# Optimization experiments

Hardware: AMD Instinct MI355X
Metric: run time of the kernel (lower is better)

The kernel has to match this reference:

```python
import jax, jax.numpy as jnp
import numpy as np

B, T, DKQ, DV, EKQ, EV, H, OUT = 8, 2048, 64, 64, 128, 128, 4, 32
FF = 4 * EV
NEG = -1e30  # additive mask value (safe stand-in for -inf)


def _ln(x, g, b, eps=1e-5):
    m = x.mean(-1, keepdims=True)
    var = ((x - m) ** 2).mean(-1, keepdims=True)
    return (x - m) * jax.lax.rsqrt(var + eps) * g + b


def _attn(q, k, v, mask):
    # q,k,v: [n, T, E] -> heads [n, H, T, dh]; NOTE: no 1/sqrt(d) scaling (faithful to source)
    n, t, _ = q.shape
    q = q.reshape(n, t, H, -1).transpose(0, 2, 1, 3)
    k = k.reshape(n, t, H, -1).transpose(0, 2, 1, 3)
    v = v.reshape(n, t, H, -1).transpose(0, 2, 1, 3)
    w = jnp.einsum('bhqd,bhkd->bhqk', q, k) + mask  # [n,H,T,T]
    a = jax.nn.softmax(w, axis=-1)
    o = jnp.einsum('bhqk,bhkd->bhqd', a, v)
    return o.transpose(0, 2, 1, 3).reshape(n, t, -1)


def setup_inputs() -> dict:
    key = jax.random.key(0)
    ks = jax.random.split(key, 32)
    w = lambda k, s: jax.random.normal(k, s, jnp.float32) * 0.02
    DIN_A = DKQ + DV
    return {
        'kq': jax.random.normal(ks[0], (B, T, DKQ), jnp.float32),
        'v': jax.random.normal(ks[1], (B, T, DV), jnp.float32),
        # Layer A (input_dim = DKQ+DV, embed = EV)
        'A_Wk': w(ks[2], (DIN_A, EV)), 'A_bk': jnp.zeros((EV,), jnp.float32),
        'A_Wq': w(ks[3], (DIN_A, EV)), 'A_bq': jnp.zeros((EV,), jnp.float32),
        'A_Wv': w(ks[4], (DIN_A, EV)), 'A_bv': jnp.zeros((EV,), jnp.float32),
        'A_f1W': w(ks[5], (EV, FF)), 'A_f1b': jnp.zeros((FF,), jnp.float32),
        'A_f2W': w(ks[6], (FF, EV)), 'A_f2b': jnp.zeros((EV,), jnp.float32),
        'A_n1g': jnp.ones((EV,), jnp.float32), 'A_n1b': jnp.zeros((EV,), jnp.float32),
        'A_n2g': jnp.ones((EV,), jnp.float32), 'A_n2b': jnp.zeros((EV,), jnp.float32),
        # Layer B (kq -> EKQ, vA -> EV)
        'B_Wk': w(ks[7], (DKQ, EKQ)), 'B_bk': jnp.zeros((EKQ,), jnp.float32),
        'B_Wq': w(ks[8], (DKQ, EKQ)), 'B_bq': jnp.zeros((EKQ,), jnp.float32),
        'B_Wv': w(ks[9], (EV, EV)), 'B_bv': jnp.zeros((EV,), jnp.float32),
        'B_f1W': w(ks[10], (EV, FF)), 'B_f1b': jnp.zeros((FF,), jnp.float32),
        'B_f2W': w(ks[11], (FF, EV)), 'B_f2b': jnp.zeros((EV,), jnp.float32),
        # Output head
        'out_W': w(ks[12], (EV, OUT)), 'out_b': jnp.zeros((OUT,), jnp.float32),
    }


def reference(kq, v, A_Wk, A_bk, A_Wq, A_bq, A_Wv, A_bv, A_f1W, A_f1b, A_f2W, A_f2b,
              A_n1g, A_n1b, A_n2g, A_n2b, B_Wk, B_bk, B_Wq, B_bq, B_Wv, B_bv,
              B_f1W, B_f1b, B_f2W, B_f2b, out_W, out_b):
    n, t, _ = kq.shape
    i = jnp.arange(t)[:, None]
    j = jnp.arange(t)[None, :]
    mask_a = jnp.where(j <= i, 0.0, NEG).astype(jnp.float32)               # causal (diag=1)
    mask_b = jnp.where((j < i) | ((i == 0) & (j == 0)), 0.0, NEG).astype(jnp.float32)  # strict causal + (0,0) exception

    # ---- Layer A ----
    X = jnp.concatenate([kq, v], axis=-1)
    K = X @ A_Wk + A_bk
    Q = X @ A_Wq + A_bq
    V = X @ A_Wv + A_bv
    attn_out = _attn(Q, K, V, mask_a)
    h1 = _ln(V + attn_out, A_n1g, A_n1b)
    ff = jax.nn.gelu(h1 @ A_f1W + A_f1b, approximate=False) @ A_f2W + A_f2b
    vA = _ln(h1 + ff, A_n2g, A_n2b)

    # ---- Layer B (no residuals / norms: values is overwritten in source) ----
    K2 = kq @ B_Wk + B_bk
    Q2 = kq @ B_Wq + B_bq
    V2 = vA @ B_Wv + B_bv
    attn_out2 = _attn(Q2, K2, V2, mask_b)
    ff2 = jax.nn.gelu(attn_out2 @ B_f1W + B_f1b, approximate=False) @ B_f2W + B_f2b

    return ff2 @ out_W + out_b
```

## Files before the change

### kernel.cpp

```cpp
#include <hip/hip_runtime.h>
#include <hip/hip_bf16.h>
#include <type_traits>

#define TSEQ 2048
#define NBATCH 8
#define NROWS (NBATCH*TSEQ)
#define EMB 128
#define NH 4
#define DH 32
#define OUTD 32
#define APLANE (NROWS*EMB)
#define LOG2E 1.44269504088896340736f
#define NPAR 4

typedef short s8v __attribute__((ext_vector_type(8)));
typedef short s4v __attribute__((ext_vector_type(4)));
typedef float f4v __attribute__((ext_vector_type(4)));
typedef float f16v __attribute__((ext_vector_type(16)));
typedef unsigned int u4v __attribute__((ext_vector_type(4)));

__device__ __forceinline__ unsigned short f2bf(float f){
  unsigned int u = __float_as_uint(f);
  unsigned int r = u + 0x7fffu + ((u >> 16) & 1u);
  return (unsigned short)(r >> 16);
}
__device__ __forceinline__ float bf2f(unsigned short u){
  return __uint_as_float(((unsigned int)u) << 16);
}
__device__ __forceinline__ float exp2fast(float x){
#if __has_builtin(__builtin_amdgcn_exp2f)
  return __builtin_amdgcn_exp2f(x);
#else
  return __expf(x * 0.6931471805599453f);
#endif
}

struct WPack {
  const float* src[10];
  int off[10];
  int ntk[10];
  int rowoff[10];
  int nsh[10];
  int kn[10];
};
__global__ __launch_bounds__(256) void prep(WPack p, short* __restrict__ warena,
                                            const float* __restrict__ kq, const float* __restrict__ v,
                                            unsigned short* __restrict__ X){
  int blk = blockIdx.x;
  if (blk < (NROWS*EMB/256)){
    int idx = blk*256 + threadIdx.x;
    int row = idx >> 7, c = idx & 127;
    float val = (c < 64) ? kq[row*64 + c] : v[row*64 + (c-64)];
    unsigned short hi = f2bf(val);
    X[idx]          = hi;
    X[idx + APLANE] = f2bf(val - bf2f(hi));
    return;
  }
  blk -= (NROWS*EMB/256);
  int m = 0;
  #pragma unroll
  for (int i=0;i<10;i++){
    int nb = p.kn[i] >> 8;
    if (blk < nb){ m = i; break; }
    blk -= nb;
  }
  int idx = blk*256 + threadIdx.x;
  float x = p.src[m][idx];
  int nsh = p.nsh[m];
  int n = idx & ((1<<nsh)-1);
  int k = idx >> nsh;
  int K = p.kn[m] >> nsh;
  unsigned short hi = f2bf(x);
  unsigned short lo = f2bf(x - bf2f(hi));
  short* dh = warena + p.off[m] + (size_t)(p.rowoff[m] + n)*K + k;
  dh[0]        = (short)hi;
  dh[p.ntk[m]] = (short)lo;
}

struct GOuts {
  const float* bias[3];
  float* of[3];
  unsigned short* ob[3];
  float scl[3];
};
template<int CT, int NWV, int NITER, int CB>
__global__ __launch_bounds__(NWV*64) void gemm2(
    const unsigned short* __restrict__ A, int aplane, int lda, int K,
    const short* __restrict__ wt, int NTK,
    GOuts og, int NT, int nseg, int act,
    unsigned short* __restrict__ vtb, int vcol0,
    const float* __restrict__ cbO, const float* __restrict__ cbL){
  __shared__ short As[2][2][64*40];
  const int tid  = threadIdx.x;
  const int w    = tid >> 6;
  const int lane = tid & 63;
  const int col  = lane & 15;
  const int quad = lane >> 4;
  const int row0 = blockIdx.x * 64;
  const int cb   = blockIdx.y*(NWV*16*CT) + w*(16*CT) + col;
  const bool two = CB ? true : (aplane != 0);

  f4v acc[4][CT];
  #pragma unroll
  for (int i=0;i<4;i++)
    #pragma unroll
    for (int j=0;j<CT;j++) acc[i][j] = (f4v){0.f,0.f,0.f,0.f};

  using sv = typename std::conditional<NWV==4, s8v, s4v>::type;
  const int ar = (NWV==4) ? (tid >> 2) : (tid >> 3);
  const int ac = (NWV==4) ? ((tid & 3)*8) : ((tid & 7)*4);

  const unsigned short* abase = nullptr;
  sv pah, pal;
  float4 cnx[NPAR]; float cnl[NPAR];
  if constexpr (CB){
    #pragma unroll
    for (int p2=0;p2<NPAR;p2++){
      cnx[p2] = *(const float4*)(cbO + (size_t)p2*NROWS*EMB + (size_t)(row0+ar)*EMB + ac);
      cnl[p2] = cbL[(size_t)p2*NROWS*NH + (size_t)(row0+ar)*NH + 0];
    }
  } else {
    abase = A + (size_t)(row0 + ar)*lda;
    pah = *(const sv*)(abase + ac);
    if (two) pal = *(const sv*)(abase + aplane + ac);
  }

  const short* wbase[CT];
  #pragma unroll
  for (int ct=0;ct<CT;ct++) wbase[ct] = wt + (size_t)(cb + ct*16)*K + quad*8;

  s8v wh[CT], wl[CT], wnh[CT], wnl[CT];
  #pragma unroll
  for (int ct=0;ct<CT;ct++){
    wh[ct] = *(const s8v*)(wbase[ct]);
    wl[ct] = *(const s8v*)(wbase[ct] + NTK);
  }

  #pragma unroll
  for (int i=0;i<NITER;i++){
    const int buf = i & 1;
    if constexpr (CB){
      float sx=0.f, sy=0.f, sz=0.f, sw=0.f, ls=0.f;
      #pragma unroll
      for (int p2=0;p2<NPAR;p2++){
        sx += cnx[p2].x; sy += cnx[p2].y; sz += cnx[p2].z; sw += cnx[p2].w;
        ls += cnl[p2];
      }
      const float linv = 1.f/ls;
      float xs[4] = {sx*linv, sy*linv, sz*linv, sw*linv};
      s4v ph, pl;
      #pragma unroll
      for (int j=0;j<4;j++){
        unsigned short hb = f2bf(xs[j]);
        ph[j] = (short)hb;
        pl[j] = (short)f2bf(xs[j] - bf2f(hb));
      }
      *(s4v*)&As[buf][0][ar*40 + ac] = ph;
      *(s4v*)&As[buf][1][ar*40 + ac] = pl;
    } else {
      *(sv*)&As[buf][0][ar*40 + ac] = pah;
      if (two) *(sv*)&As[buf][1][ar*40 + ac] = pal;
    }
    __syncthreads();
    if (i+1 < NITER){
      if constexpr (CB){
        #pragma unroll
        for (int p2=0;p2<NPAR;p2++){
          cnx[p2] = *(const float4*)(cbO + (size_t)p2*NROWS*EMB + (size_t)(row0+ar)*EMB + (i+1)*32 + ac);
          cnl[p2] = cbL[(size_t)p2*NROWS*NH + (size_t)(row0+ar)*NH + (i+1)];
        }
      } else {
        const int kcol = (i+1)*32 + ac;
        pah = *(const sv*)(abase + kcol);
        if (two) pal = *(const sv*)(abase + aplane + kcol);
      }
      #pragma unroll
      for (int ct=0;ct<CT;ct++){
        wnh[ct] = *(const s8v*)(wbase[ct] + (i+1)*32);
        wnl[ct] = *(const s8v*)(wbase[ct] + (i+1)*32 + NTK);
      }
    }
    #pragma unroll
    for (int rt=0;rt<4;rt++){
      s8v ah = *(const s8v*)&As[buf][0][(rt*16 + col)*40 + quad*8];
      #pragma unroll
      for (int ct=0;ct<CT;ct++)
        acc[rt][ct] = __builtin_amdgcn_mfma_f32_16x16x32_bf16(ah, wh[ct], acc[rt][ct], 0, 0, 0);
      if (two){
        s8v al = *(const s8v*)&As[buf][1][(rt*16 + col)*40 + quad*8];
        #pragma unroll
        for (int ct=0;ct<CT;ct++)
          acc[rt][ct] = __builtin_amdgcn_mfma_f32_16x16x32_bf16(al, wh[ct], acc[rt][ct], 0, 0, 0);
      }
      #pragma unroll
      for (int ct=0;ct<CT;ct++)
        acc[rt][ct] = __builtin_amdgcn_mfma_f32_16x16x32_bf16(ah, wl[ct], acc[rt][ct], 0, 0, 0);
    }
    if (i+1 < NITER){
      #pragma unroll
      for (int ct=0;ct<CT;ct++){ wh[ct] = wnh[ct]; wl[ct] = wnl[ct]; }
    }
  }

  const int NB = NWV*16*CT;
  const int cb0 = (int)blockIdx.y * NB;
  const bool dotr = (NB == 128) && (vtb != nullptr) && (cb0 >= vcol0) && (cb0 < vcol0 + 128);
  short* Lt = &As[0][0][0];
  if (dotr) __syncthreads();

  #pragma unroll
  for (int ct=0;ct<CT;ct++){
    const int cg = cb + ct*16;
    int seg, lcol, ldc;
    if (nseg > 1){ seg = cg >> 7; lcol = cg & 127; ldc = 128; }
    else         { seg = 0; lcol = cg; ldc = NT; }
    const float bv = og.bias[seg][lcol];
    const float sc = og.scl[seg];
    float* of = og.of[seg];
    unsigned short* ob = og.ob[seg];
    #pragma unroll
    for (int rt=0;rt<4;rt++){
      s4v pk;
      #pragma unroll
      for (int r=0;r<4;r++){
        const int row = row0 + rt*16 + quad*4 + r;
        float val = acc[rt][ct][r] + bv;
        if (act == 1) val = 0.5f*val*(1.f + erff(val*0.70710678118654752440f));
        val *= sc;
        if (ob)      ob[(size_t)row*ldc + lcol] = f2bf(val);
        else if (of) of[(size_t)row*ldc + lcol] = val;
        if (dotr) pk[r] = (short)f2bf(val);
      }
      if (dotr)
        *(s4v*)&Lt[((cg - cb0))*72 + rt*16 + quad*4] = pk;
    }
  }
  if (dotr){
    __syncthreads();
    const int b = row0 >> 11, t0 = row0 & 2047;
    #pragma unroll
    for (int it=0; it<2*CT; it++){
      const int cl = it*(NWV*8) + (tid>>3);
      const int t8 = (tid&7)*8;
      s8v o = *(const s8v*)&Lt[cl*72 + t8];
      const int cr = cb0 + cl - vcol0;
      *(s8v*)(vtb + ((size_t)((b*4 + (cr>>5))*32 + (cr&31)))*2048 + t0 + t8) = o;
    }
  }
}

template<int MODE>
__global__ __launch_bounds__(512) void gemm_f2(
    const unsigned short* __restrict__ A,
    const short* __restrict__ wt, int NTK,
    const float* __restrict__ bias,
    const unsigned short* __restrict__ resid,
    const float* __restrict__ g, const float* __restrict__ bt,
    unsigned short* __restrict__ outp,
    const float* __restrict__ Wo, const float* __restrict__ bo,
    float* __restrict__ outhead){
  __shared__ short As[2][64*40];
  __shared__ float Lf[64*132];
  __shared__ float Ws2[128*32];
  const int tid  = threadIdx.x;
  const int w    = tid >> 6;
  const int lane = tid & 63;
  const int col  = lane & 15;
  const int quad = lane >> 4;
  const int row0 = blockIdx.x * 64;
  const int cg   = w*16 + col;

  if (MODE == 1){
    for (int idx = tid; idx < 128*32; idx += 512) Ws2[idx] = Wo[idx];
  }

  f4v acc[4];
  #pragma unroll
  for (int i=0;i<4;i++) acc[i] = (f4v){0.f,0.f,0.f,0.f};

  const int ar = tid >> 3, ac = (tid & 7)*4;
  const unsigned short* abase = A + (size_t)(row0 + ar)*512;
  s4v pa = *(const s4v*)(abase + ac);
  const short* wb = wt + (size_t)cg*512 + quad*8;

  for (int i=0;i<16;i++){
    const int buf = i & 1;
    *(s4v*)&As[buf][ar*40 + ac] = pa;
    __syncthreads();
    if (i+1 < 16) pa = *(const s4v*)(abase + (i+1)*32 + ac);
    s8v bh = *(const s8v*)(wb + i*32);
    s8v bl = *(const s8v*)(wb + i*32 + NTK);
    #pragma unroll
    for (int rt=0;rt<4;rt++){
      s8v ah = *(const s8v*)&As[buf][(rt*16 + col)*40 + quad*8];
      acc[rt] = __builtin_amdgcn_mfma_f32_16x16x32_bf16(ah, bh, acc[rt], 0, 0, 0);
      acc[rt] = __builtin_amdgcn_mfma_f32_16x16x32_bf16(ah, bl, acc[rt], 0, 0, 0);
    }
  }

  const float bv = bias[cg];
  #pragma unroll
  for (int rt=0;rt<4;rt++){
    #pragma unroll
    for (int r=0;r<4;r++){
      const int row = rt*16 + quad*4 + r;
      Lf[row*132 + cg] = acc[rt][r] + bv;
    }
  }
  __syncthreads();

  if (MODE == 0){
    for (int rr=0; rr<8; rr++){
      const int row = w*8 + rr;
      const size_t gbase = (size_t)(row0 + row)*EMB;
      float x0 = Lf[row*132 + lane]
               + bf2f(resid[gbase+lane])    + bf2f(resid[gbase+lane+APLANE]);
      float x1 = Lf[row*132 + lane + 64]
               + bf2f(resid[gbase+lane+64]) + bf2f(resid[gbase+lane+64+APLANE]);
      float s  = x0 + x1;
      float s2 = x0*x0 + x1*x1;
      #pragma unroll
      for (int off=1; off<64; off<<=1){
        s  += __shfl_xor(s,  off);
        s2 += __shfl_xor(s2, off);
      }
      float mean = s * (1.f/128.f);
      float var  = s2 * (1.f/128.f) - mean*mean;
      float rstd = rsqrtf(var + 1e-5f);
      float y0 = (x0-mean)*rstd*g[lane]    + bt[lane];
      float y1 = (x1-mean)*rstd*g[lane+64] + bt[lane+64];
      unsigned short h0b = f2bf(y0), h1b = f2bf(y1);
      outp[gbase+lane]             = h0b;
      outp[gbase+lane+64]          = h1b;
      outp[gbase+lane+APLANE]      = f2bf(y0 - bf2f(h0b));
      outp[gbase+lane+64+APLANE]   = f2bf(y1 - bf2f(h1b));
    }
  } else {
    const int row = tid >> 3, c0 = (tid & 7)*4;
    f4v a4;
    #pragma unroll
    for (int j=0;j<4;j++) a4[j] = bo[c0+j];
    #pragma unroll 16
    for (int k=0;k<128;k++){
      const float av = Lf[row*132 + k];
      #pragma unroll
      for (int j=0;j<4;j++) a4[j] = fmaf(av, Ws2[k*32 + c0 + j], a4[j]);
    }
    float* op = outhead + (size_t)(row0 + row)*OUTD + c0;
    #pragma unroll
    for (int j=0;j<4;j++) op[j] = a4[j];
  }
}

#define KSTR 40
#define VSTR 72
__device__ __forceinline__ int kswz(int row, int c){ return (row*KSTR + c) ^ (((row>>3)&3)<<3); }
__device__ __forceinline__ int vswz(int row, int c){ return (row*VSTR + c) ^ (((row>>3)&3)<<3); }

__global__ __launch_bounds__(256, 4) void flash5(const unsigned short* __restrict__ Qb,
                                                 const unsigned short* __restrict__ Kb,
                                                 const unsigned short* __restrict__ Vtb,
                                                 float* __restrict__ O, float* __restrict__ L,
                                                 int mode){
  __shared__ short Kt[64*KSTR];
  __shared__ short Vt[32*VSTR];
  const int tid  = threadIdx.x;
  const int w    = tid >> 6;
  const int lane = tid & 63;
  const int q31  = lane & 31;
  const int hi   = lane >> 5;
  const int bh = blockIdx.y;
  const int b = bh >> 2, h = bh & 3;
  const int par = blockIdx.z;
  float* Op = O + (size_t)par*NROWS*EMB;
  float* Lp = L + (size_t)par*NROWS*NH;
  const int kr = tid >> 2, kc8 = (tid & 3)*8;
  const int vd = tid >> 3, vk8 = (tid & 7)*8;

  for (int pass = 0; pass < 2; pass++){
    const int qt = pass ? (int)blockIdx.x : (15 - (int)blockIdx.x);
    const int qbase = qt*128;
    const int qrow  = qbase + w*32 + q31;
    const int jtmax = 2*qt + 1;

    s8v qB0 = *(const s8v*)(Qb + (size_t)(b*TSEQ + qrow)*EMB + h*DH + hi*8);
    s8v qB1 = *(const s8v*)(Qb + (size_t)(b*TSEQ + qrow)*EMB + h*DH + 16 + hi*8);
    f16v o;
    #pragma unroll
    for (int r=0;r<16;r++) o[r] = 0.f;
    float lr = 0.f;

    if (par <= jtmax){
      s8v ka = *(const s8v*)(Kb + (size_t)(b*TSEQ + par*64 + kr)*EMB + h*DH + kc8);
      s8v va = *(const s8v*)(Vtb + ((size_t)bh*32 + vd)*TSEQ + par*64 + vk8);
      for (int jt = par; jt <= jtmax; jt += NPAR){
        __syncthreads();
        *(s8v*)&Kt[kswz(kr, kc8)] = ka;
        *(s8v*)&Vt[vswz(vd, vk8)] = va;
        __syncthreads();
        if (jt + NPAR <= jtmax){
          ka = *(const s8v*)(Kb + (size_t)(b*TSEQ + (jt+NPAR)*64 + kr)*EMB + h*DH + kc8);
          va = *(const s8v*)(Vtb + ((size_t)bh*32 + vd)*TSEQ + (jt+NPAR)*64 + vk8);
        }
        const bool domask = (jt >= 2*qt);
        #pragma unroll
        for (int kt=0;kt<2;kt++){
          f16v s;
          #pragma unroll
          for (int r=0;r<16;r++) s[r] = 0.f;
          {
            s8v kf0 = *(const s8v*)&Kt[kswz(kt*32 + q31, hi*8)];
            s = __builtin_amdgcn_mfma_f32_32x32x16_bf16(kf0, qB0, s, 0, 0, 0);
            s8v kf1 = *(const s8v*)&Kt[kswz(kt*32 + q31, 16 + hi*8)];
            s = __builtin_amdgcn_mfma_f32_32x32x16_bf16(kf1, qB1, s, 0, 0, 0);
          }
          if (domask){
            #pragma unroll
            for (int r=0;r<16;r++){
              const int jg = jt*64 + kt*32 + (r&3) + 8*(r>>2) + 4*hi;
              const bool ok = (mode==0) ? (jg <= qrow) : ((jg < qrow) || (qrow==0 && jg==0));
              s[r] = ok ? s[r] : -1e30f;
            }
          }
          #pragma unroll
          for (int r=0;r<16;r++){ float pv = exp2fast(s[r]); s[r] = pv; lr += pv; }
          unsigned P2[4][2];
          #pragma unroll
          for (int m=0;m<4;m++){
            asm("v_cvt_pk_bf16_f32 %0, %1, %2" : "=v"(P2[m][0]) : "v"(s[4*m+0]), "v"(s[4*m+1]));
            asm("v_cvt_pk_bf16_f32 %0, %1, %2" : "=v"(P2[m][1]) : "v"(s[4*m+2]), "v"(s[4*m+3]));
          }
          #pragma unroll
          for (int kcl=0;kcl<2;kcl++){
            const unsigned own0 = hi ? P2[2*kcl+1][0] : P2[2*kcl][0];
            const unsigned own1 = hi ? P2[2*kcl+1][1] : P2[2*kcl][1];
            const unsigned inv0 = hi ? P2[2*kcl][0]   : P2[2*kcl+1][0];
            const unsigned inv1 = hi ? P2[2*kcl][1]   : P2[2*kcl+1][1];
            const unsigned sx0 = (unsigned)__shfl_xor((int)inv0, 32);
            const unsigned sx1 = (unsigned)__shfl_xor((int)inv1, 32);
            u4v au;
            au[0] = hi ? sx0 : own0;  au[1] = hi ? sx1 : own1;
            au[2] = hi ? own0 : sx0;  au[3] = hi ? own1 : sx1;
            s8v af = __builtin_bit_cast(s8v, au);
            s8v vf = *(const s8v*)&Vt[vswz(q31, kt*32 + kcl*16 + hi*8)];
            o = __builtin_amdgcn_mfma_f32_32x32x16_bf16(af, vf, o, 0, 0, 0);
          }
        }
      }
    }
    const float lt = lr + __shfl_xor(lr, 32);
    #pragma unroll
    for (int r=0;r<16;r++){
      const int ql = (r&3) + 8*(r>>2) + 4*hi;
      Op[(size_t)(b*TSEQ + qbase + w*32 + ql)*EMB + h*DH + q31] = o[r];
    }
    if (hi == 0) Lp[(size_t)(b*TSEQ + qrow)*NH + h] = lt;
  }
}

__global__ __launch_bounds__(256) void combine_ln(const float* __restrict__ O, const float* __restrict__ L,
                                                  const float* __restrict__ Vf,
                                                  const float* __restrict__ g, const float* __restrict__ bt,
                                                  unsigned short* __restrict__ outp){
  const int row = blockIdx.x*4 + (threadIdx.x >> 6);
  const int tid = threadIdx.x & 63;
  const size_t base = (size_t)row*EMB;
  const int h0 = tid >> 5, h1i = 2 + (tid >> 5);
  float la = 0.f, lb = 0.f, s0 = 0.f, s1 = 0.f;
  #pragma unroll
  for (int p=0;p<NPAR;p++){
    la += L[(size_t)p*NROWS*NH + (size_t)row*NH + h0];
    lb += L[(size_t)p*NROWS*NH + (size_t)row*NH + h1i];
    s0 += O[(size_t)p*NROWS*EMB + base + tid];
    s1 += O[(size_t)p*NROWS*EMB + base + tid + 64];
  }
  float x0 = Vf[base+tid]    + s0/la;
  float x1 = Vf[base+tid+64] + s1/lb;
  float s  = x0 + x1;
  float s2 = x0*x0 + x1*x1;
  #pragma unroll
  for (int off=1; off<64; off<<=1){
    s  += __shfl_xor(s,  off);
    s2 += __shfl_xor(s2, off);
  }
  float mean = s * (1.f/128.f);
  float var  = s2 * (1.f/128.f) - mean*mean;
  float rstd = rsqrtf(var + 1e-5f);
  float y0 = (x0-mean)*rstd*g[tid]    + bt[tid];
  float y1 = (x1-mean)*rstd*g[tid+64] + bt[tid+64];
  unsigned short h0b = f2bf(y0), h1b = f2bf(y1);
  outp[base+tid]             = h0b;
  outp[base+tid+64]          = h1b;
  outp[base+tid+APLANE]      = f2bf(y0 - bf2f(h0b));
  outp[base+tid+64+APLANE]   = f2bf(y1 - bf2f(h1b));
}

extern "C" void kernel_launch(void* const* d_in, const int* in_sizes, int n_in,
                              void* d_out, int out_size, void* d_ws, size_t ws_size,
                              hipStream_t stream) {
  const float* kq    = (const float*)d_in[0];
  const float* v     = (const float*)d_in[1];
  const float* A_Wk  = (const float*)d_in[2];  const float* A_bk  = (const float*)d_in[3];
  const float* A_Wq  = (const float*)d_in[4];  const float* A_bq  = (const float*)d_in[5];
  const float* A_Wv  = (const float*)d_in[6];  const float* A_bv  = (const float*)d_in[7];
  const float* A_f1W = (const float*)d_in[8];  const float* A_f1b = (const float*)d_in[9];
  const float* A_f2W = (const float*)d_in[10]; const float* A_f2b = (const float*)d_in[11];
  const float* A_n1g = (const float*)d_in[12]; const float* A_n1b = (const float*)d_in[13];
  const float* A_n2g = (const float*)d_in[14]; const float* A_n2b = (const float*)d_in[15];
  const float* B_Wk  = (const float*)d_in[16]; const float* B_bk  = (const float*)d_in[17];
  const float* B_Wq  = (const float*)d_in[18]; const float* B_bq  = (const float*)d_in[19];
  const float* B_Wv  = (const float*)d_in[20]; const float* B_bv  = (const float*)d_in[21];
  const float* B_f1W = (const float*)d_in[22]; const float* B_f1b = (const float*)d_in[23];
  const float* B_f2W = (const float*)d_in[24]; const float* B_f2b = (const float*)d_in[25];
  const float* out_W = (const float*)d_in[26]; const float* out_b = (const float*)d_in[27];
  float* out = (float*)d_out;
  (void)in_sizes; (void)n_in; (void)out_size; (void)ws_size;

  char* ws = (char*)d_ws;
  const size_t MB = 1024*1024;
  short* warena = (short*)ws;
  unsigned short* Xs  = (unsigned short*)(ws + 2*MB);
  unsigned short* Qbf = (unsigned short*)(ws + 10*MB);
  unsigned short* Kbf = (unsigned short*)(ws + 14*MB);
  unsigned short* Vtb = (unsigned short*)(ws + 18*MB);
  float* Vf  = (float*)(ws + 22*MB);
  float* Opar = (float*)(ws + 30*MB);
  float* Lpar = (float*)(ws + 62*MB);
  unsigned short* h1p = (unsigned short*)(ws + 66*MB);
  unsigned short* mid = (unsigned short*)(ws + 74*MB);
  unsigned short* vAp = (unsigned short*)(ws + 90*MB);

  WPack p;
  const float* srcs[10] = {A_Wq,A_Wk,A_Wv,A_f1W,A_f2W,B_Wq,B_Wk,B_Wv,B_f1W,B_f2W};
  int kn[10]     = {16384,16384,16384,65536,65536,8192,8192,16384,65536,65536};
  int nsh[10]    = {7,7,7,9,7,7,7,7,9,7};
  int off[10]    = {0,0,0,98304,229376,360448,360448,393216,425984,557056};
  int ntk[10]    = {49152,49152,49152,65536,65536,16384,16384,16384,65536,65536};
  int rowoff[10] = {0,128,256,0,0,0,128,0,0,0};
  int nblk = 0;
  for (int i=0;i<10;i++){
    p.src[i]=srcs[i]; p.kn[i]=kn[i]; p.nsh[i]=nsh[i];
    p.off[i]=off[i]; p.ntk[i]=ntk[i]; p.rowoff[i]=rowoff[i];
    nblk += kn[i] >> 8;
  }
  prep<<<(NROWS*EMB/256) + nblk, 256, 0, stream>>>(p, warena, kq, v, Xs);

  GOuts oQKVA = {{A_bq,A_bk,A_bv},{nullptr,nullptr,Vf},{Qbf,Kbf,nullptr},{LOG2E,1.f,1.f}};
  GOuts oF1A  = {{A_f1b,nullptr,nullptr},{nullptr,nullptr,nullptr},{mid,nullptr,nullptr},{1.f,1.f,1.f}};
  GOuts oQKB  = {{B_bq,B_bk,nullptr},{nullptr,nullptr,nullptr},{Qbf,Kbf,nullptr},{LOG2E,1.f,1.f}};
  GOuts oVB   = {{B_bv,nullptr,nullptr},{nullptr,nullptr,nullptr},{nullptr,nullptr,nullptr},{1.f,1.f,1.f}};
  GOuts oF1B  = {{B_f1b,nullptr,nullptr},{nullptr,nullptr,nullptr},{mid,nullptr,nullptr},{1.f,1.f,1.f}};

  gemm2<2,4,4,0><<<dim3(256,3), 256, 0, stream>>>(Xs, APLANE, 128, 128, warena + 0, 49152, oQKVA, 384, 3, 0, Vtb, 256, nullptr, nullptr);
  flash5<<<dim3(8,32,NPAR), 256, 0, stream>>>(Qbf, Kbf, Vtb, Opar, Lpar, 0);
  combine_ln<<<NROWS/4, 256, 0, stream>>>(Opar, Lpar, Vf, A_n1g, A_n1b, h1p);
  gemm2<2,8,4,0><<<dim3(256,2), 512, 0, stream>>>(h1p, APLANE, 128, 128, warena + 98304, 65536, oF1A, 512, 1, 1, nullptr, 0, nullptr, nullptr);
  gemm_f2<0><<<256, 512, 0, stream>>>(mid, warena + 229376, 65536, A_f2b,
                                      h1p, A_n2g, A_n2b, vAp, nullptr, nullptr, nullptr);

  gemm2<2,8,2,0><<<dim3(256,1), 512, 0, stream>>>(Xs, APLANE, 128, 64, warena + 360448, 16384, oQKB, 256, 2, 0, nullptr, 0, nullptr, nullptr);
  gemm2<1,8,4,0><<<dim3(256,1), 512, 0, stream>>>(vAp, APLANE, 128, 128, warena + 393216, 16384, oVB, 128, 1, 0, Vtb, 0, nullptr, nullptr);
  flash5<<<dim3(8,32,NPAR), 256, 0, stream>>>(Qbf, Kbf, Vtb, Opar, Lpar, 1);
  gemm2<2,8,4,1><<<dim3(256,2), 512, 0, stream>>>(nullptr, 1, 128, 128, warena + 425984, 65536, oF1B, 512, 1, 1, nullptr, 0, Opar, Lpar);
  gemm_f2<1><<<256, 512, 0, stream>>>(mid, warena + 557056, 65536, B_f2b,
                                      nullptr, nullptr, nullptr, nullptr, out_W, out_b, out);
}
```

Measured before the change: 274.3 us.

## Fuse attention combine+LayerNorm into FF1 GEMM and merge QKV launches

Removes the separate combine_ln kernel by computing the partial-attention combine, residual add and LayerNorm inside the FF1 GEMM prologue (new CB==2 mode), with the by==0 blocks also writing h1 for the later residual. It also merges layer A's QKV GEMM and layer B's QK GEMM into a single launch, using separate Q/K buffers so layer B's projections don't overwrite layer A's. This cuts two kernel launches and one round trip of h1 through memory. The cost is that both column blocks of the FF1 GEMM redundantly redo the combine and LayerNorm reads, and register pressure in the prologue goes up.

```diff
diff --git a/kernel.cpp b/kernel.cpp
--- a/kernel.cpp
+++ b/kernel.cpp
@@ -83,22 +83,26 @@
   unsigned short* ob[3];
   float scl[3];
 };
+struct GArgs {
+  const unsigned short* A; int aplane; int lda; int K;
+  const short* wt; int NTK;
+  GOuts og; int NT; int nseg; int act;
+  unsigned short* vtb; int vcol0;
+  const float* cbO; const float* cbL;
+  const float* vf; const float* lng; const float* lnb;
+  unsigned short* h1out;
+};
+
 template<int CT, int NWV, int NITER, int CB>
-__global__ __launch_bounds__(NWV*64) void gemm2(
-    const unsigned short* __restrict__ A, int aplane, int lda, int K,
-    const short* __restrict__ wt, int NTK,
-    GOuts og, int NT, int nseg, int act,
-    unsigned short* __restrict__ vtb, int vcol0,
-    const float* __restrict__ cbO, const float* __restrict__ cbL){
-  __shared__ short As[2][2][64*40];
+__device__ __forceinline__ void gemm2_body(short* __restrict__ AsD, const GArgs a, int bx, int by){
   const int tid  = threadIdx.x;
   const int w    = tid >> 6;
   const int lane = tid & 63;
   const int col  = lane & 15;
   const int quad = lane >> 4;
-  const int row0 = blockIdx.x * 64;
-  const int cb   = blockIdx.y*(NWV*16*CT) + w*(16*CT) + col;
-  const bool two = CB ? true : (aplane != 0);
+  const int row0 = bx * 64;
+  const int cb   = by*(NWV*16*CT) + w*(16*CT) + col;
+  const bool two = (CB != 0) ? true : (a.aplane != 0);
 
   f4v acc[4][CT];
   #pragma unroll
@@ -113,33 +117,69 @@
   const unsigned short* abase = nullptr;
   sv pah, pal;
   float4 cnx[NPAR]; float cnl[NPAR];
-  if constexpr (CB){
+  float x[16];
+  if constexpr (CB == 1){
     #pragma unroll
     for (int p2=0;p2<NPAR;p2++){
-      cnx[p2] = *(const float4*)(cbO + (size_t)p2*NROWS*EMB + (size_t)(row0+ar)*EMB + ac);
-      cnl[p2] = cbL[(size_t)p2*NROWS*NH + (size_t)(row0+ar)*NH + 0];
-    }
+      cnx[p2] = *(const float4*)(a.cbO + (size_t)p2*NROWS*EMB + (size_t)(row0+ar)*EMB + ac);
+      cnl[p2] = a.cbL[(size_t)p2*NROWS*NH + (size_t)(row0+ar)*NH + 0];
+    }
+  } else if constexpr (CB == 2){
+    float s = 0.f, s2 = 0.f;
+    #pragma unroll
+    for (int i=0;i<NITER;i++){
+      float sx=0.f, sy=0.f, sz=0.f, sw=0.f, ls=0.f;
+      #pragma unroll
+      for (int p2=0;p2<NPAR;p2++){
+        float4 t = *(const float4*)(a.cbO + (size_t)p2*NROWS*EMB + (size_t)(row0+ar)*EMB + i*32 + ac);
+        sx += t.x; sy += t.y; sz += t.z; sw += t.w;
+        ls += a.cbL[(size_t)p2*NROWS*NH + (size_t)(row0+ar)*NH + i];
+      }
+      float4 vv = *(const float4*)(a.vf + (size_t)(row0+ar)*EMB + i*32 + ac);
+      const float linv = 1.f/ls;
+      x[i*4+0] = vv.x + sx*linv;
+      x[i*4+1] = vv.y + sy*linv;
+      x[i*4+2] = vv.z + sz*linv;
+      x[i*4+3] = vv.w + sw*linv;
+      #pragma unroll
+      for (int j=0;j<4;j++){ s += x[i*4+j]; s2 += x[i*4+j]*x[i*4+j]; }
+    }
+    #pragma unroll
+    for (int off=1; off<8; off<<=1){
+      s  += __shfl_xor(s,  off);
+      s2 += __shfl_xor(s2, off);
+    }
+    const float mean = s * (1.f/128.f);
+    const float var  = s2 * (1.f/128.f) - mean*mean;
+    const float rstd = rsqrtf(var + 1e-5f);
+    #pragma unroll
+    for (int i=0;i<NITER;i++)
+      #pragma unroll
+      for (int j=0;j<4;j++){
+        const int cg2 = i*32 + ac + j;
+        x[i*4+j] = (x[i*4+j]-mean)*rstd*a.lng[cg2] + a.lnb[cg2];
+      }
   } else {
-    abase = A + (size_t)(row0 + ar)*lda;
+    abase = a.A + (size_t)(row0 + ar)*a.lda;
     pah = *(const sv*)(abase + ac);
-    if (two) pal = *(const sv*)(abase + aplane + ac);
+    if (two) pal = *(const sv*)(abase + a.aplane + ac);
   }
 
   const short* wbase[CT];
   #pragma unroll
-  for (int ct=0;ct<CT;ct++) wbase[ct] = wt + (size_t)(cb + ct*16)*K + quad*8;
+  for (int ct=0;ct<CT;ct++) wbase[ct] = a.wt + (size_t)(cb + ct*16)*a.K + quad*8;
 
   s8v wh[CT], wl[CT], wnh[CT], wnl[CT];
   #pragma unroll
   for (int ct=0;ct<CT;ct++){
     wh[ct] = *(const s8v*)(wbase[ct]);
-    wl[ct] = *(const s8v*)(wbase[ct] + NTK);
+    wl[ct] = *(const s8v*)(wbase[ct] + a.NTK);
   }
 
   #pragma unroll
   for (int i=0;i<NITER;i++){
     const int buf = i & 1;
-    if constexpr (CB){
+    if constexpr (CB == 1){
       float sx=0.f, sy=0.f, sz=0.f, sw=0.f, ls=0.f;
       #pragma unroll
       for (int p2=0;p2<NPAR;p2++){
@@ -155,39 +195,53 @@
         ph[j] = (short)hb;
         pl[j] = (short)f2bf(xs[j] - bf2f(hb));
       }
-      *(s4v*)&As[buf][0][ar*40 + ac] = ph;
-      *(s4v*)&As[buf][1][ar*40 + ac] = pl;
+      *(s4v*)&AsD[(buf*2+0)*2560 + ar*40 + ac] = ph;
+      *(s4v*)&AsD[(buf*2+1)*2560 + ar*40 + ac] = pl;
+    } else if constexpr (CB == 2){
+      s4v ph, pl;
+      #pragma unroll
+      for (int j=0;j<4;j++){
+        unsigned short hb = f2bf(x[i*4+j]);
+        ph[j] = (short)hb;
+        pl[j] = (short)f2bf(x[i*4+j] - bf2f(hb));
+      }
+      *(s4v*)&AsD[(buf*2+0)*2560 + ar*40 + ac] = ph;
+      *(s4v*)&AsD[(buf*2+1)*2560 + ar*40 + ac] = pl;
+      if (by == 0 && a.h1out){
+        *(s4v*)(a.h1out + (size_t)(row0+ar)*EMB + i*32 + ac) = ph;
+        *(s4v*)(a.h1out + APLANE + (size_t)(row0+ar)*EMB + i*32 + ac) = pl;
+      }
     } else {
-      *(sv*)&As[buf][0][ar*40 + ac] = pah;
-      if (two) *(sv*)&As[buf][1][ar*40 + ac] = pal;
+      *(sv*)&AsD[(buf*2+0)*2560 + ar*40 + ac] = pah;
+      if (two) *(sv*)&AsD[(buf*2+1)*2560 + ar*40 + ac] = pal;
     }
     __syncthreads();
     if (i+1 < NITER){
-      if constexpr (CB){
+      if constexpr (CB == 1){
         #pragma unroll
         for (int p2=0;p2<NPAR;p2++){
-          cnx[p2] = *(const float4*)(cbO + (size_t)p2*NROWS*EMB + (size_t)(row0+ar)*EMB + (i+1)*32 + ac);
-          cnl[p2] = cbL[(size_t)p2*NROWS*NH + (size_t)(row0+ar)*NH + (i+1)];
+          cnx[p2] = *(const float4*)(a.cbO + (size_t)p2*NROWS*EMB + (size_t)(row0+ar)*EMB + (i+1)*32 + ac);
+          cnl[p2] = a.cbL[(size_t)p2*NROWS*NH + (size_t)(row0+ar)*NH + (i+1)];
         }
-      } else {
+      } else if constexpr (CB == 0){
         const int kcol = (i+1)*32 + ac;
         pah = *(const sv*)(abase + kcol);
-        if (two) pal = *(const sv*)(abase + aplane + kcol);
+        if (two) pal = *(const sv*)(abase + a.aplane + kcol);
       }
       #pragma unroll
       for (int ct=0;ct<CT;ct++){
         wnh[ct] = *(const s8v*)(wbase[ct] + (i+1)*32);
-        wnl[ct] = *(const s8v*)(wbase[ct] + (i+1)*32 + NTK);
+        wnl[ct] = *(const s8v*)(wbase[ct] + (i+1)*32 + a.NTK);
       }
     }
     #pragma unroll
     for (int rt=0;rt<4;rt++){
-      s8v ah = *(const s8v*)&As[buf][0][(rt*16 + col)*40 + quad*8];
+      s8v ah = *(const s8v*)&AsD[(buf*2+0)*2560 + (rt*16 + col)*40 + quad*8];
       #pragma unroll
       for (int ct=0;ct<CT;ct++)
         acc[rt][ct] = __builtin_amdgcn_mfma_f32_16x16x32_bf16(ah, wh[ct], acc[rt][ct], 0, 0, 0);
       if (two){
-        s8v al = *(const s8v*)&As[buf][1][(rt*16 + col)*40 + quad*8];
+        s8v al = *(const s8v*)&AsD[(buf*2+1)*2560 + (rt*16 + col)*40 + quad*8];
         #pragma unroll
         for (int ct=0;ct<CT;ct++)
           acc[rt][ct] = __builtin_amdgcn_mfma_f32_16x16x32_bf16(al, wh[ct], acc[rt][ct], 0, 0, 0);
@@ -203,21 +257,21 @@
   }
 
   const int NB = NWV*16*CT;
-  const int cb0 = (int)blockIdx.y * NB;
-  const bool dotr = (NB == 128) && (vtb != nullptr) && (cb0 >= vcol0) && (cb0 < vcol0 + 128);
-  short* Lt = &As[0][0][0];
+  const int cb0 = by * NB;
+  const bool dotr = (NB == 128) && (a.vtb != nullptr) && (cb0 >= a.vcol0) && (cb0 < a.vcol0 + 128);
+  short* Lt = AsD;
   if (dotr) __syncthreads();
 
   #pragma unroll
   for (int ct=0;ct<CT;ct++){
     const int cg = cb + ct*16;
     int seg, lcol, ldc;
-    if (nseg > 1){ seg = cg >> 7; lcol = cg & 127; ldc = 128; }
-    else         { seg = 0; lcol = cg; ldc = NT; }
-    const float bv = og.bias[seg][lcol];
-    const float sc = og.scl[seg];
-    float* of = og.of[seg];
-    unsigned short* ob = og.ob[seg];
+    if (a.nseg > 1){ seg = cg >> 7; lcol = cg & 127; ldc = 128; }
+    else           { seg = 0; lcol = cg; ldc = a.NT; }
+    const float bv = a.og.bias[seg][lcol];
+    const float sc = a.og.scl[seg];
+    float* of = a.og.of[seg];
+    unsigned short* ob = a.og.ob[seg];
     #pragma unroll
     for (int rt=0;rt<4;rt++){
       s4v pk;
@@ -225,7 +279,7 @@
       for (int r=0;r<4;r++){
         const int row = row0 + rt*16 + quad*4 + r;
         float val = acc[rt][ct][r] + bv;
-        if (act == 1) val = 0.5f*val*(1.f + erff(val*0.70710678118654752440f));
+        if (a.act == 1) val = 0.5f*val*(1.f + erff(val*0.70710678118654752440f));
         val *= sc;
         if (ob)      ob[(size_t)row*ldc + lcol] = f2bf(val);
         else if (of) of[(size_t)row*ldc + lcol] = val;
@@ -243,10 +297,22 @@
       const int cl = it*(NWV*8) + (tid>>3);
       const int t8 = (tid&7)*8;
       s8v o = *(const s8v*)&Lt[cl*72 + t8];
-      const int cr = cb0 + cl - vcol0;
-      *(s8v*)(vtb + ((size_t)((b*4 + (cr>>5))*32 + (cr&31)))*2048 + t0 + t8) = o;
-    }
-  }
+      const int cr = cb0 + cl - a.vcol0;
+      *(s8v*)(a.vtb + ((size_t)((b*4 + (cr>>5))*32 + (cr&31)))*2048 + t0 + t8) = o;
+    }
+  }
+}
+
+template<int CT, int NWV, int NITER, int CB>
+__global__ __launch_bounds__(NWV*64) void gemm2k(GArgs a){
+  extern __shared__ short AsD[];
+  gemm2_body<CT,NWV,NITER,CB>(AsD, a, blockIdx.x, blockIdx.y);
+}
+
+__global__ __launch_bounds__(256) void gemm_mixa(GArgs qkva, GArgs qkb){
+  extern __shared__ short AsD[];
+  if (blockIdx.y < 3) gemm2_body<2,4,4,0>(AsD, qkva, blockIdx.x, blockIdx.y);
+  else                gemm2_body<2,4,2,0>(AsD, qkb,  blockIdx.x, blockIdx.y - 3);
 }
 
 template<int MODE>
@@ -458,43 +524,6 @@
   }
 }
 
-__global__ __launch_bounds__(256) void combine_ln(const float* __restrict__ O, const float* __restrict__ L,
-                                                  const float* __restrict__ Vf,
-                                                  const float* __restrict__ g, const float* __restrict__ bt,
-                                                  unsigned short* __restrict__ outp){
-  const int row = blockIdx.x*4 + (threadIdx.x >> 6);
-  const int tid = threadIdx.x & 63;
-  const size_t base = (size_t)row*EMB;
-  const int h0 = tid >> 5, h1i = 2 + (tid >> 5);
-  float la = 0.f, lb = 0.f, s0 = 0.f, s1 = 0.f;
-  #pragma unroll
-  for (int p=0;p<NPAR;p++){
-    la += L[(size_t)p*NROWS*NH + (size_t)row*NH + h0];
-    lb += L[(size_t)p*NROWS*NH + (size_t)row*NH + h1i];
-    s0 += O[(size_t)p*NROWS*EMB + base + tid];
-    s1 += O[(size_t)p*NROWS*EMB + base + tid + 64];
-  }
-  float x0 = Vf[base+tid]    + s0/la;
-  float x1 = Vf[base+tid+64] + s1/lb;
-  float s  = x0 + x1;
-  float s2 = x0*x0 + x1*x1;
-  #pragma unroll
-  for (int off=1; off<64; off<<=1){
-    s  += __shfl_xor(s,  off);
-    s2 += __shfl_xor(s2, off);
-  }
-  float mean = s * (1.f/128.f);
-  float var  = s2 * (1.f/128.f) - mean*mean;
-  float rstd = rsqrtf(var + 1e-5f);
-  float y0 = (x0-mean)*rstd*g[tid]    + bt[tid];
-  float y1 = (x1-mean)*rstd*g[tid+64] + bt[tid+64];
-  unsigned short h0b = f2bf(y0), h1b = f2bf(y1);
-  outp[base+tid]             = h0b;
-  outp[base+tid+64]          = h1b;
-  outp[base+tid+APLANE]      = f2bf(y0 - bf2f(h0b));
-  outp[base+tid+64+APLANE]   = f2bf(y1 - bf2f(h1b));
-}
-
 extern "C" void kernel_launch(void* const* d_in, const int* in_sizes, int n_in,
                               void* d_out, int out_size, void* d_ws, size_t ws_size,
                               hipStream_t stream) {
@@ -529,6 +558,8 @@
   unsigned short* h1p = (unsigned short*)(ws + 66*MB);
   unsigned short* mid = (unsigned short*)(ws + 74*MB);
   unsigned short* vAp = (unsigned short*)(ws + 90*MB);
+  unsigned short* Qb2 = (unsigned short*)(ws + 98*MB);
+  unsigned short* Kb2 = (unsigned short*)(ws + 102*MB);
 
   WPack p;
   const float* srcs[10] = {A_Wq,A_Wk,A_Wv,A_f1W,A_f2W,B_Wq,B_Wk,B_Wv,B_f1W,B_f2W};
@@ -547,21 +578,27 @@
 
   GOuts oQKVA = {{A_bq,A_bk,A_bv},{nullptr,nullptr,Vf},{Qbf,Kbf,nullptr},{LOG2E,1.f,1.f}};
   GOuts oF1A  = {{A_f1b,nullptr,nullptr},{nullptr,nullptr,nullptr},{mid,nullptr,nullptr},{1.f,1.f,1.f}};
-  GOuts oQKB  = {{B_bq,B_bk,nullptr},{nullptr,nullptr,nullptr},{Qbf,Kbf,nullptr},{LOG2E,1.f,1.f}};
+  GOuts oQKB  = {{B_bq,B_bk,nullptr},{nullptr,nullptr,nullptr},{Qb2,Kb2,nullptr},{LOG2E,1.f,1.f}};
   GOuts oVB   = {{B_bv,nullptr,nullptr},{nullptr,nullptr,nullptr},{nullptr,nullptr,nullptr},{1.f,1.f,1.f}};
   GOuts oF1B  = {{B_f1b,nullptr,nullptr},{nullptr,nullptr,nullptr},{mid,nullptr,nullptr},{1.f,1.f,1.f}};
 
-  gemm2<2,4,4,0><<<dim3(256,3), 256, 0, stream>>>(Xs, APLANE, 128, 128, warena + 0, 49152, oQKVA, 384, 3, 0, Vtb, 256, nullptr, nullptr);
+  const int SH = 2*2*64*40*(int)sizeof(short);
+
+  GArgs aQKVA = {Xs, APLANE, 128, 128, warena + 0,      49152, oQKVA, 384, 3, 0, Vtb, 256, nullptr, nullptr, nullptr, nullptr, nullptr, nullptr};
+  GArgs aQKB  = {Xs, APLANE, 128, 64,  warena + 360448, 16384, oQKB,  256, 2, 0, nullptr, 0, nullptr, nullptr, nullptr, nullptr, nullptr, nullptr};
+  GArgs aF1A  = {nullptr, 1, 128, 128, warena + 98304,  65536, oF1A,  512, 1, 1, nullptr, 0, Opar, Lpar, Vf, A_n1g, A_n1b, h1p};
+  GArgs aVB   = {vAp, APLANE, 128, 128, warena + 393216, 16384, oVB,  128, 1, 0, Vtb, 0, nullptr, nullptr, nullptr, nullptr, nullptr, nullptr};
+  GArgs aF1B  = {nullptr, 1, 128, 128, warena + 425984,  65536, oF1B,  512, 1, 1, nullptr, 0, Opar, Lpar, nullptr, nullptr, nullptr, nullptr};
+
+  gemm_mixa<<<dim3(256,5), 256, SH, stream>>>(aQKVA, aQKB);
   flash5<<<dim3(8,32,NPAR), 256, 0, stream>>>(Qbf, Kbf, Vtb, Opar, Lpar, 0);
-  combine_ln<<<NROWS/4, 256, 0, stream>>>(Opar, Lpar, Vf, A_n1g, A_n1b, h1p);
-  gemm2<2,8,4,0><<<dim3(256,2), 512, 0, stream>>>(h1p, APLANE, 128, 128, warena + 98304, 65536, oF1A, 512, 1, 1, nullptr, 0, nullptr, nullptr);
+  gemm2k<2,8,4,2><<<dim3(256,2), 512, SH, stream>>>(aF1A);
   gemm_f2<0><<<256, 512, 0, stream>>>(mid, warena + 229376, 65536, A_f2b,
                                       h1p, A_n2g, A_n2b, vAp, nullptr, nullptr, nullptr);
 
-  gemm2<2,8,2,0><<<dim3(256,1), 512, 0, stream>>>(Xs, APLANE, 128, 64, warena + 360448, 16384, oQKB, 256, 2, 0, nullptr, 0, nullptr, nullptr);
-  gemm2<1,8,4,0><<<dim3(256,1), 512, 0, stream>>>(vAp, APLANE, 128, 128, warena + 393216, 16384, oVB, 128, 1, 0, Vtb, 0, nullptr, nullptr);
-  flash5<<<dim3(8,32,NPAR), 256, 0, stream>>>(Qbf, Kbf, Vtb, Opar, Lpar, 1);
-  gemm2<2,8,4,1><<<dim3(256,2), 512, 0, stream>>>(nullptr, 1, 128, 128, warena + 425984, 65536, oF1B, 512, 1, 1, nullptr, 0, Opar, Lpar);
+  gemm2k<1,8,4,0><<<dim3(256,1), 512, SH, stream>>>(aVB);
+  flash5<<<dim3(8,32,NPAR), 256, 0, stream>>>(Qb2, Kb2, Vtb, Opar, Lpar, 1);
+  gemm2k<2,8,4,1><<<dim3(256,2), 512, SH, stream>>>(aF1B);
   gemm_f2<1><<<256, 512, 0, stream>>>(mid, warena + 557056, 65536, B_f2b,
                                       nullptr, nullptr, nullptr, nullptr, out_W, out_b, out);
 }
```

Result: no change. 279.5 us (+1.9%).
